# Kernel tuning notes

Measured on AMD Instinct MI355X. Metric: run time of the kernel, lower is better.

## Reference

```python
import jax, jax.numpy as jnp
import numpy as np

B, S, D, H = 4, 2048, 1024, 16
HD = D // H


def setup_inputs() -> dict:
    key = jax.random.key(0)
    ks = jax.random.split(key, 11)
    s = 1.0 / np.sqrt(D)
    return {
        "query": jax.random.normal(ks[0], (B, S, D), jnp.float32),
        "key": jax.random.normal(ks[1], (B, S, D), jnp.float32),
        "value": jax.random.normal(ks[2], (B, S, D), jnp.float32),
        "Wq": jax.random.normal(ks[3], (D, D), jnp.float32) * s,
        "bq": jax.random.normal(ks[4], (D,), jnp.float32) * s,
        "Wk": jax.random.normal(ks[5], (D, D), jnp.float32) * s,
        "bk": jax.random.normal(ks[6], (D,), jnp.float32) * s,
        "Wv": jax.random.normal(ks[7], (D, D), jnp.float32) * s,
        "bv": jax.random.normal(ks[8], (D,), jnp.float32) * s,
        "Wo": jax.random.normal(ks[9], (D, D), jnp.float32) * s,
        "bo": jax.random.normal(ks[10], (D,), jnp.float32) * s,
    }


def reference(query, key, value, Wq, bq, Wk, bk, Wv, bv, Wo, bo):
    b = query.shape[0]
    # projections (torch Linear: x @ W.T + b)
    q = (query @ Wq.T + bq).reshape(b, -1, H, HD).transpose(0, 2, 1, 3)  # [B,H,S,hd]
    k = (key @ Wk.T + bk).reshape(b, -1, H, HD).transpose(0, 2, 1, 3)
    v = (value @ Wv.T + bv).reshape(b, -1, H, HD).transpose(0, 2, 1, 3)
    scores = jnp.einsum('bhqd,bhkd->bhqk', q, k) / jnp.sqrt(jnp.float32(HD))
    attn = jax.nn.softmax(scores, axis=-1)  # dropout = identity (eval)
    out = jnp.einsum('bhqk,bhkd->bhqd', attn, v)
    out = out.transpose(0, 2, 1, 3).reshape(b, -1, D)
    return out @ Wo.T + bo
```

## Files before the change

### kernel.cpp

```cpp
#include <hip/hip_runtime.h>
#include <stdint.h>

typedef __attribute__((ext_vector_type(8))) short  s16x8;
typedef __attribute__((ext_vector_type(4))) float  f32x4;
typedef __attribute__((ext_vector_type(4))) unsigned short u16x4;

__device__ __forceinline__ unsigned short f2bf(float f) {
  union { float f; uint32_t u; } x; x.f = f;
  uint32_t u = x.u;
  return (unsigned short)((u + 0x7fffu + ((u >> 16) & 1u)) >> 16);
}

__device__ __forceinline__ float fexp2(float x) {
  float r; asm("v_exp_f32 %0, %1" : "=v"(r) : "v"(x)); return r;
}
__device__ __forceinline__ uint32_t cvtpk_bf16(float lo, float hi) {
  uint32_t r; asm("v_cvt_pk_bf16_f32 %0, %1, %2" : "=v"(r) : "v"(lo), "v"(hi)); return r;
}

__device__ __forceinline__ void gload_lds16(const void* g, void* l) {
  __builtin_amdgcn_global_load_lds(
      (const __attribute__((address_space(1))) void*)g,
      (__attribute__((address_space(3))) void*)l, 16, 0, 0);
}

struct CvtJobs {
  const float* src[7];
  unsigned short* dst[7];
  int n4[7];
};
__global__ __launch_bounds__(256) void cvt_all(CvtJobs jobs) {
  const int j = blockIdx.y;
  const float* __restrict__ src = jobs.src[j];
  unsigned short* __restrict__ dst = jobs.dst[j];
  const int n4 = jobs.n4[j];
  const int stride = gridDim.x * blockDim.x;
  for (int i = blockIdx.x * blockDim.x + threadIdx.x; i < n4; i += stride) {
    f32x4 v = *(const f32x4*)(src + (size_t)i * 4);
    u16x4 o = { f2bf(v[0]), f2bf(v[1]), f2bf(v[2]), f2bf(v[3]) };
    *(u16x4*)(dst + (size_t)i * 4) = o;
  }
}

struct GemmJob {
  const unsigned short* A;
  const unsigned short* Bmat;
  const float* bias;
  unsigned short* C;
  int M, N, Nb;
  int bias_row;
  float scale;
};

__device__ __forceinline__ void gemm_core(const unsigned short* __restrict__ A,
                                          const unsigned short* __restrict__ Bw,
                                          int m0, int n0, int K,
                                          unsigned short* Al, unsigned short* Bl,
                                          f32x4 (&acc)[4][4]) {
  const int tid = threadIdx.x;
  const int l = tid & 63, w = tid >> 6;
  const int lr = l & 15, lc = l >> 4;
  const int wr = w >> 1, wc = w & 1;
  const int srow = l >> 2, skc = (l & 3) * 8;
  for (int kt = 0; kt < K; kt += 32) {
#pragma unroll
    for (int p = 0; p < 2; ++p) {
      int c = w + 4 * p;
      int row = c * 16 + srow;
      gload_lds16(A + (size_t)(m0 + row) * K + kt + skc, &Al[c * 512 + l * 8]);
      gload_lds16(Bw + (size_t)(n0 + row) * K + kt + skc, &Bl[c * 512 + l * 8]);
    }
    __syncthreads();
    s16x8 af[4], bfr[4];
#pragma unroll
    for (int i = 0; i < 4; ++i)
      af[i] = *(const s16x8*)&Al[(wr * 64 + i * 16 + lr) * 32 + lc * 8];
#pragma unroll
    for (int j = 0; j < 4; ++j)
      bfr[j] = *(const s16x8*)&Bl[(wc * 64 + j * 16 + lr) * 32 + lc * 8];
#pragma unroll
    for (int i = 0; i < 4; ++i)
#pragma unroll
      for (int j = 0; j < 4; ++j)
        acc[i][j] = __builtin_amdgcn_mfma_f32_16x16x32_bf16(af[i], bfr[j], acc[i][j], 0, 0, 0);
    __syncthreads();
  }
}

__global__ __launch_bounds__(256) void gemm_qkv(GemmJob j0, GemmJob j1, GemmJob j2) {
  __shared__ __align__(16) unsigned short Al[4096];
  __shared__ __align__(16) unsigned short Bl[4096];
  const GemmJob jb = (blockIdx.y == 0) ? j0 : (blockIdx.y == 1) ? j1 : j2;
  const int flat = blockIdx.x;
  const int m0 = (flat / jb.Nb) * 128, n0 = (flat % jb.Nb) * 128;
  f32x4 acc[4][4];
#pragma unroll
  for (int i = 0; i < 4; ++i)
#pragma unroll
    for (int j = 0; j < 4; ++j) acc[i][j] = (f32x4){0.f, 0.f, 0.f, 0.f};
  gemm_core(jb.A, jb.Bmat, m0, n0, 1024, Al, Bl, acc);
  const int tid = threadIdx.x;
  const int l = tid & 63, w = tid >> 6;
  const int lr = l & 15, lc = l >> 4;
  const int wr = w >> 1, wc = w & 1;
#pragma unroll
  for (int i = 0; i < 4; ++i) {
    const int row0 = m0 + wr * 64 + i * 16 + lc * 4;
    f32x4 brow;
    if (jb.bias_row) brow = *(const f32x4*)&jb.bias[row0];
#pragma unroll
    for (int j = 0; j < 4; ++j) {
      const int col = n0 + wc * 64 + j * 16 + lr;
      float bcol = jb.bias_row ? 0.f : jb.bias[col];
#pragma unroll
      for (int r = 0; r < 4; ++r) {
        float v = (acc[i][j][r] + (jb.bias_row ? brow[r] : bcol)) * jb.scale;
        jb.C[(size_t)(row0 + r) * jb.N + col] = f2bf(v);
      }
    }
  }
}

__global__ __launch_bounds__(256) void gemm_out(const unsigned short* __restrict__ A,
                                                const unsigned short* __restrict__ Bw,
                                                const float* __restrict__ bias,
                                                float* __restrict__ Cout,
                                                int M, int N, int K) {
  __shared__ __align__(16) unsigned short Al[4096];
  __shared__ __align__(16) unsigned short Bl[4096];
  const int m0 = blockIdx.x * 128, n0 = blockIdx.y * 128;
  f32x4 acc[4][4];
#pragma unroll
  for (int i = 0; i < 4; ++i)
#pragma unroll
    for (int j = 0; j < 4; ++j) acc[i][j] = (f32x4){0.f, 0.f, 0.f, 0.f};
  gemm_core(A, Bw, m0, n0, K, Al, Bl, acc);
  const int tid = threadIdx.x;
  const int l = tid & 63, w = tid >> 6;
  const int lr = l & 15, lc = l >> 4;
  const int wr = w >> 1, wc = w & 1;
#pragma unroll
  for (int i = 0; i < 4; ++i) {
    const int row0 = m0 + wr * 64 + i * 16 + lc * 4;
#pragma unroll
    for (int j = 0; j < 4; ++j) {
      const int col = n0 + wc * 64 + j * 16 + lr;
      float bcol = bias[col];
#pragma unroll
      for (int r = 0; r < 4; ++r)
        Cout[(size_t)(row0 + r) * N + col] = acc[i][j][r] + bcol;
    }
  }
}

__global__ __launch_bounds__(512) void attn_fwd(const unsigned short* __restrict__ qb,
                                                const unsigned short* __restrict__ kb,
                                                const unsigned short* __restrict__ vtb,
                                                unsigned short* __restrict__ ob) {
  __shared__ __align__(16) unsigned short L[3 * 8192];
  const int tid = threadIdx.x;
  const int l = tid & 63, w = tid >> 6;
  const int lr = l & 15, lc = l >> 4;
  const int i0 = blockIdx.x;
  const int wid = (i0 & 7) * 128 + (i0 >> 3);
  const int qx = wid & 15;
  const int h = (wid >> 4) & 15;
  const int b = wid >> 8;
  const int q0 = qx * 128;
  const size_t qkbase = ((size_t)b * 2048) * 1024 + (size_t)h * 64;
  const size_t vtbase = (size_t)(h * 64) * 8192 + (size_t)b * 2048;

  s16x8 aq0, aq1;
  {
    const unsigned short* qp = qb + qkbase + (size_t)(q0 + w * 16 + lr) * 1024 + lc * 8;
    aq0 = *(const s16x8*)qp;
    aq1 = *(const s16x8*)(qp + 32);
  }

  float lsum = 0.f;
  f32x4 oacc[4];
#pragma unroll
  for (int nd = 0; nd < 4; ++nd) oacc[nd] = (f32x4){0.f, 0.f, 0.f, 0.f};

  const int role = w >> 2, wk = w & 3;
  const int rl = l >> 3;
  const int cs = (l & 7) ^ rl;
  const int rA = wk * 16 + rl, rB = rA + 8;
#define RHO(rr) (8 * (((rr) >> 2) & 3) + 4 * (((rr) >> 4) & 1) + ((rr) & 3) + 32 * ((rr) >> 5))
  const unsigned short* sA;
  const unsigned short* sB;
  size_t tstep;
  if (role == 0) {
    sA = kb + qkbase + (size_t)RHO(rA) * 1024 + cs * 8;
    sB = kb + qkbase + (size_t)RHO(rB) * 1024 + cs * 8;
    tstep = (size_t)64 * 1024;
  } else {
    sA = vtb + vtbase + (size_t)rA * 8192 + cs * 8;
    sB = vtb + vtbase + (size_t)rB * 8192 + cs * 8;
    tstep = 64;
  }
#undef RHO
  char* dstL = (char*)L + role * 8192 + wk * 2048 + l * 16;

#define STAGE(BUF, T) {                                              \
    gload_lds16(sA + (size_t)(T) * tstep, dstL + (BUF) * 16384);     \
    gload_lds16(sB + (size_t)(T) * tstep, dstL + (BUF) * 16384 + 1024); }

  int off0[4];
#pragma unroll
  for (int ni = 0; ni < 4; ++ni)
    off0[ni] = (ni * 16 + lr) * 128 + ((lc ^ (lr & 7)) * 16);

  STAGE(0, 0);
  STAGE(1, 1);

  int cur = 0;
  for (int t = 0; t < 32; ++t) {
    if (t < 31) asm volatile("s_waitcnt vmcnt(2)" ::: "memory");
    else        asm volatile("s_waitcnt vmcnt(0)" ::: "memory");
    __builtin_amdgcn_s_barrier();
    if (t < 30) {
      int nb = cur + 2; if (nb >= 3) nb -= 3;
      STAGE(nb, t + 2);
    }
    const char* Lb = (const char*)L + cur * 16384;

    f32x4 sf[4];
    __builtin_amdgcn_s_setprio(1);
#pragma unroll
    for (int ni = 0; ni < 4; ++ni) {
      s16x8 k0 = *(const s16x8*)(Lb + off0[ni]);
      s16x8 k1 = *(const s16x8*)(Lb + (off0[ni] ^ 64));
      f32x4 z = (f32x4){0.f, 0.f, 0.f, 0.f};
      z = __builtin_amdgcn_mfma_f32_16x16x32_bf16(k0, aq0, z, 0, 0, 0);
      z = __builtin_amdgcn_mfma_f32_16x16x32_bf16(k1, aq1, z, 0, 0, 0);
      sf[ni] = z;
    }
    __builtin_amdgcn_s_setprio(0);

    union { uint32_t u[4]; s16x8 v; } pa0u, pa1u;
#pragma unroll
    for (int ni = 0; ni < 4; ++ni) {
      float p0 = fexp2(sf[ni][0]);
      float p1 = fexp2(sf[ni][1]);
      float p2 = fexp2(sf[ni][2]);
      float p3 = fexp2(sf[ni][3]);
      lsum += (p0 + p1) + (p2 + p3);
      uint32_t w0 = cvtpk_bf16(p0, p1);
      uint32_t w1 = cvtpk_bf16(p2, p3);
      if (ni < 2) { pa0u.u[ni * 2] = w0; pa0u.u[ni * 2 + 1] = w1; }
      else        { pa1u.u[(ni - 2) * 2] = w0; pa1u.u[(ni - 2) * 2 + 1] = w1; }
    }

    __builtin_amdgcn_s_setprio(1);
#pragma unroll
    for (int nd = 0; nd < 4; ++nd) {
      s16x8 v0 = *(const s16x8*)(Lb + 8192 + off0[nd]);
      s16x8 v1 = *(const s16x8*)(Lb + 8192 + (off0[nd] ^ 64));
      oacc[nd] = __builtin_amdgcn_mfma_f32_16x16x32_bf16(pa0u.v, v0, oacc[nd], 0, 0, 0);
      oacc[nd] = __builtin_amdgcn_mfma_f32_16x16x32_bf16(pa1u.v, v1, oacc[nd], 0, 0, 0);
    }
    __builtin_amdgcn_s_setprio(0);

    ++cur; if (cur == 3) cur = 0;
  }

  lsum += __shfl_xor(lsum, 16, 64);
  lsum += __shfl_xor(lsum, 32, 64);
  float linv[4];
#pragma unroll
  for (int r = 0; r < 4; ++r) linv[r] = 1.f / __shfl(lsum, lc * 4 + r, 64);
#pragma unroll
  for (int nd = 0; nd < 4; ++nd)
#pragma unroll
    for (int r = 0; r < 4; ++r) {
      int qrow = q0 + w * 16 + lc * 4 + r;
      ob[qkbase + (size_t)qrow * 1024 + nd * 16 + lr] = f2bf(oacc[nd][r] * linv[r]);
    }
#undef STAGE
}

extern "C" void kernel_launch(void* const* d_in, const int* in_sizes, int n_in,
                              void* d_out, int out_size, void* d_ws, size_t ws_size,
                              hipStream_t stream) {
  const float* query = (const float*)d_in[0];
  const float* key_  = (const float*)d_in[1];
  const float* value = (const float*)d_in[2];
  const float* Wq = (const float*)d_in[3];
  const float* bq = (const float*)d_in[4];
  const float* Wk = (const float*)d_in[5];
  const float* bk = (const float*)d_in[6];
  const float* Wv = (const float*)d_in[7];
  const float* bv = (const float*)d_in[8];
  const float* Wo = (const float*)d_in[9];
  const float* bo = (const float*)d_in[10];

  const int MS = 4 * 2048;
  const int D = 1024;
  const size_t NX = (size_t)MS * D;
  const size_t NW = (size_t)D * D;

  const size_t need = (6 * NX + 4 * NW) * 2;
  if (ws_size < need) return;

  unsigned short* ws  = (unsigned short*)d_ws;
  unsigned short* xq  = ws;
  unsigned short* xk  = xq + NX;
  unsigned short* xv  = xk + NX;
  unsigned short* qb_ = xv + NX;
  unsigned short* kb_ = qb_ + NX;
  unsigned short* vtb = kb_ + NX;
  unsigned short* wqb = vtb + NX;
  unsigned short* wkb = wqb + NW;
  unsigned short* wvb = wkb + NW;
  unsigned short* wob = wvb + NW;
  unsigned short* attn = xq;

  CvtJobs cj;
  cj.src[0] = query; cj.dst[0] = xq;  cj.n4[0] = (int)(NX / 4);
  cj.src[1] = key_;  cj.dst[1] = xk;  cj.n4[1] = (int)(NX / 4);
  cj.src[2] = value; cj.dst[2] = xv;  cj.n4[2] = (int)(NX / 4);
  cj.src[3] = Wq;    cj.dst[3] = wqb; cj.n4[3] = (int)(NW / 4);
  cj.src[4] = Wk;    cj.dst[4] = wkb; cj.n4[4] = (int)(NW / 4);
  cj.src[5] = Wv;    cj.dst[5] = wvb; cj.n4[5] = (int)(NW / 4);
  cj.src[6] = Wo;    cj.dst[6] = wob; cj.n4[6] = (int)(NW / 4);
  cvt_all<<<dim3(1024, 7), 256, 0, stream>>>(cj);

  const float qscale = 0.18033688f;
  GemmJob jq = { xq,  wqb, bq, qb_, MS, D,  D / 128,  0, qscale };
  GemmJob jk = { xk,  wkb, bk, kb_, MS, D,  D / 128,  0, 1.f };
  GemmJob jv = { wvb, xv,  bv, vtb, D,  MS, MS / 128, 1, 1.f };
  gemm_qkv<<<dim3(512, 3), 256, 0, stream>>>(jq, jk, jv);

  attn_fwd<<<dim3(1024), 512, 0, stream>>>(qb_, kb_, vtb, attn);

  gemm_out<<<dim3(MS / 128, D / 128), 256, 0, stream>>>(attn, wob, bo, (float*)d_out, MS, D, D);
}
```

Baseline: 215.4 us.

## Pipeline GEMMs with triple-buffered LDS, 8 waves, swizzle and XCD-aware block remap

Replaces the single-buffered, double-barrier GEMM core with a three-stage LDS ring in which global-to-LDS loads for tile t+2 are issued while tile t is computed, using vmcnt waits and one barrier per step. Blocks now have 512 threads (8 waves, each computing a 32x64 sub-tile), the LDS rows are XOR-swizzled to avoid bank conflicts, MFMA sections run at raised priority, and block indices are remapped across the 8 XCDs for cache locality. The intent is to hide memory latency and reduce barrier stalls in the QKV and output projections. In exchange, LDS use rises to 48KB per block and per-wave arithmetic intensity drops.

Measured after the change: 205.4 us. -4.7%, faster.

```diff
diff --git a/kernel.cpp b/kernel.cpp
--- a/kernel.cpp
+++ b/kernel.cpp
@@ -52,96 +52,121 @@
   float scale;
 };
 
-__device__ __forceinline__ void gemm_core(const unsigned short* __restrict__ A,
-                                          const unsigned short* __restrict__ Bw,
-                                          int m0, int n0, int K,
-                                          unsigned short* Al, unsigned short* Bl,
-                                          f32x4 (&acc)[4][4]) {
+__device__ __forceinline__ void gemm_core8(const unsigned short* __restrict__ A,
+                                           const unsigned short* __restrict__ Bw,
+                                           int m0, int n0, int K, char* L,
+                                           f32x4 (&acc)[2][4]) {
+  const int tid = threadIdx.x;
+  const int l = tid & 63;
+  const int lr = l & 15, lc = l >> 4;
+  const int w = tid >> 6;
+  const int wr = w >> 1, wc = w & 1;
+
+  const int srow = tid >> 2;
+  const int sc = (tid & 3) ^ ((srow >> 1) & 3);
+  const unsigned short* sA = A + (size_t)(m0 + srow) * K + sc * 8;
+  const unsigned short* sB = Bw + (size_t)(n0 + srow) * K + sc * 8;
+  char* dA = L + (size_t)tid * 16;
+  char* dB = L + 8192 + (size_t)tid * 16;
+
+#define GSTAGE(BUF, KS) { gload_lds16(sA + (KS), dA + (BUF) * 16384); \
+                          gload_lds16(sB + (KS), dB + (BUF) * 16384); }
+
+  const int s16 = (lc ^ ((lr >> 1) & 3)) * 16;
+  int offA[2], offB[4];
+#pragma unroll
+  for (int i = 0; i < 2; ++i) offA[i] = (wr * 32 + i * 16 + lr) * 64 + s16;
+#pragma unroll
+  for (int j = 0; j < 4; ++j) offB[j] = 8192 + (wc * 64 + j * 16 + lr) * 64 + s16;
+
+  const int nk = K >> 5;
+  GSTAGE(0, 0);
+  GSTAGE(1, 32);
+  int cur = 0;
+  for (int t = 0; t < nk; ++t) {
+    if (t < nk - 1) asm volatile("s_waitcnt vmcnt(2)" ::: "memory");
+    else            asm volatile("s_waitcnt vmcnt(0)" ::: "memory");
+    __builtin_amdgcn_s_barrier();
+    if (t < nk - 2) {
+      int nb = cur + 2; if (nb >= 3) nb -= 3;
+      GSTAGE(nb, (t + 2) * 32);
+    }
+    const char* Lb = L + cur * 16384;
+    s16x8 af[2], bfr[4];
+#pragma unroll
+    for (int i = 0; i < 2; ++i) af[i] = *(const s16x8*)(Lb + offA[i]);
+#pragma unroll
+    for (int j = 0; j < 4; ++j) bfr[j] = *(const s16x8*)(Lb + offB[j]);
+    __builtin_amdgcn_s_setprio(1);
+#pragma unroll
+    for (int i = 0; i < 2; ++i)
+#pragma unroll
+      for (int j = 0; j < 4; ++j)
+        acc[i][j] = __builtin_amdgcn_mfma_f32_16x16x32_bf16(af[i], bfr[j], acc[i][j], 0, 0, 0);
+    __builtin_amdgcn_s_setprio(0);
+    ++cur; if (cur == 3) cur = 0;
+  }
+#undef GSTAGE
+}
+
+__global__ __launch_bounds__(512) void gemm_qkv(GemmJob j0, GemmJob j1, GemmJob j2) {
+  __shared__ __align__(16) char L[49152];
+  const int f = blockIdx.x;
+  const int wid = (f & 7) * 192 + (f >> 3);
+  const int job = wid >> 9;
+  const int i = wid & 511;
+  const GemmJob jb = (job == 0) ? j0 : (job == 1) ? j1 : j2;
+  const int m0 = (i / jb.Nb) * 128, n0 = (i % jb.Nb) * 128;
+  f32x4 acc[2][4];
+#pragma unroll
+  for (int i2 = 0; i2 < 2; ++i2)
+#pragma unroll
+    for (int j2 = 0; j2 < 4; ++j2) acc[i2][j2] = (f32x4){0.f, 0.f, 0.f, 0.f};
+  gemm_core8(jb.A, jb.Bmat, m0, n0, 1024, L, acc);
   const int tid = threadIdx.x;
   const int l = tid & 63, w = tid >> 6;
   const int lr = l & 15, lc = l >> 4;
   const int wr = w >> 1, wc = w & 1;
-  const int srow = l >> 2, skc = (l & 3) * 8;
-  for (int kt = 0; kt < K; kt += 32) {
-#pragma unroll
-    for (int p = 0; p < 2; ++p) {
-      int c = w + 4 * p;
-      int row = c * 16 + srow;
-      gload_lds16(A + (size_t)(m0 + row) * K + kt + skc, &Al[c * 512 + l * 8]);
-      gload_lds16(Bw + (size_t)(n0 + row) * K + kt + skc, &Bl[c * 512 + l * 8]);
-    }
-    __syncthreads();
-    s16x8 af[4], bfr[4];
-#pragma unroll
-    for (int i = 0; i < 4; ++i)
-      af[i] = *(const s16x8*)&Al[(wr * 64 + i * 16 + lr) * 32 + lc * 8];
-#pragma unroll
-    for (int j = 0; j < 4; ++j)
-      bfr[j] = *(const s16x8*)&Bl[(wc * 64 + j * 16 + lr) * 32 + lc * 8];
-#pragma unroll
-    for (int i = 0; i < 4; ++i)
-#pragma unroll
-      for (int j = 0; j < 4; ++j)
-        acc[i][j] = __builtin_amdgcn_mfma_f32_16x16x32_bf16(af[i], bfr[j], acc[i][j], 0, 0, 0);
-    __syncthreads();
-  }
-}
-
-__global__ __launch_bounds__(256) void gemm_qkv(GemmJob j0, GemmJob j1, GemmJob j2) {
-  __shared__ __align__(16) unsigned short Al[4096];
-  __shared__ __align__(16) unsigned short Bl[4096];
-  const GemmJob jb = (blockIdx.y == 0) ? j0 : (blockIdx.y == 1) ? j1 : j2;
-  const int flat = blockIdx.x;
-  const int m0 = (flat / jb.Nb) * 128, n0 = (flat % jb.Nb) * 128;
-  f32x4 acc[4][4];
-#pragma unroll
-  for (int i = 0; i < 4; ++i)
+#pragma unroll
+  for (int i2 = 0; i2 < 2; ++i2) {
+    const int row0 = m0 + wr * 32 + i2 * 16 + lc * 4;
+    f32x4 brow;
+    if (jb.bias_row) brow = *(const f32x4*)&jb.bias[row0];
+#pragma unroll
+    for (int j2 = 0; j2 < 4; ++j2) {
+      const int col = n0 + wc * 64 + j2 * 16 + lr;
+      float bcol = jb.bias_row ? 0.f : jb.bias[col];
+#pragma unroll
+      for (int r = 0; r < 4; ++r) {
+        float v = (acc[i2][j2][r] + (jb.bias_row ? brow[r] : bcol)) * jb.scale;
+        jb.C[(size_t)(row0 + r) * jb.N + col] = f2bf(v);
+      }
+    }
+  }
+}
+
+__global__ __launch_bounds__(512) void gemm_out(const unsigned short* __restrict__ A,
+                                                const unsigned short* __restrict__ Bw,
+                                                const float* __restrict__ bias,
+                                                float* __restrict__ Cout,
+                                                int M, int N, int K) {
+  __shared__ __align__(16) char L[49152];
+  const int f = blockIdx.x;
+  const int wid = (f & 7) * 64 + (f >> 3);
+  const int m0 = (wid >> 3) * 128, n0 = (wid & 7) * 128;
+  f32x4 acc[2][4];
+#pragma unroll
+  for (int i = 0; i < 2; ++i)
 #pragma unroll
     for (int j = 0; j < 4; ++j) acc[i][j] = (f32x4){0.f, 0.f, 0.f, 0.f};
-  gemm_core(jb.A, jb.Bmat, m0, n0, 1024, Al, Bl, acc);
+  gemm_core8(A, Bw, m0, n0, K, L, acc);
   const int tid = threadIdx.x;
   const int l = tid & 63, w = tid >> 6;
   const int lr = l & 15, lc = l >> 4;
   const int wr = w >> 1, wc = w & 1;
 #pragma unroll
-  for (int i = 0; i < 4; ++i) {
-    const int row0 = m0 + wr * 64 + i * 16 + lc * 4;
-    f32x4 brow;
-    if (jb.bias_row) brow = *(const f32x4*)&jb.bias[row0];
-#pragma unroll
-    for (int j = 0; j < 4; ++j) {
-      const int col = n0 + wc * 64 + j * 16 + lr;
-      float bcol = jb.bias_row ? 0.f : jb.bias[col];
-#pragma unroll
-      for (int r = 0; r < 4; ++r) {
-        float v = (acc[i][j][r] + (jb.bias_row ? brow[r] : bcol)) * jb.scale;
-        jb.C[(size_t)(row0 + r) * jb.N + col] = f2bf(v);
-      }
-    }
-  }
-}
-
-__global__ __launch_bounds__(256) void gemm_out(const unsigned short* __restrict__ A,
-                                                const unsigned short* __restrict__ Bw,
-                                                const float* __restrict__ bias,
-                                                float* __restrict__ Cout,
-                                                int M, int N, int K) {
-  __shared__ __align__(16) unsigned short Al[4096];
-  __shared__ __align__(16) unsigned short Bl[4096];
-  const int m0 = blockIdx.x * 128, n0 = blockIdx.y * 128;
-  f32x4 acc[4][4];
-#pragma unroll
-  for (int i = 0; i < 4; ++i)
-#pragma unroll
-    for (int j = 0; j < 4; ++j) acc[i][j] = (f32x4){0.f, 0.f, 0.f, 0.f};
-  gemm_core(A, Bw, m0, n0, K, Al, Bl, acc);
-  const int tid = threadIdx.x;
-  const int l = tid & 63, w = tid >> 6;
-  const int lr = l & 15, lc = l >> 4;
-  const int wr = w >> 1, wc = w & 1;
-#pragma unroll
-  for (int i = 0; i < 4; ++i) {
-    const int row0 = m0 + wr * 64 + i * 16 + lc * 4;
+  for (int i = 0; i < 2; ++i) {
+    const int row0 = m0 + wr * 32 + i * 16 + lc * 4;
 #pragma unroll
     for (int j = 0; j < 4; ++j) {
       const int col = n0 + wc * 64 + j * 16 + lr;
@@ -330,9 +355,9 @@
   GemmJob jq = { xq,  wqb, bq, qb_, MS, D,  D / 128,  0, qscale };
   GemmJob jk = { xk,  wkb, bk, kb_, MS, D,  D / 128,  0, 1.f };
   GemmJob jv = { wvb, xv,  bv, vtb, D,  MS, MS / 128, 1, 1.f };
-  gemm_qkv<<<dim3(512, 3), 256, 0, stream>>>(jq, jk, jv);
+  gemm_qkv<<<dim3(1536), 512, 0, stream>>>(jq, jk, jv);
 
   attn_fwd<<<dim3(1024), 512, 0, stream>>>(qb_, kb_, vtb, attn);
 
-  gemm_out<<<dim3(MS / 128, D / 128), 256, 0, stream>>>(attn, wob, bo, (float*)d_out, MS, D, D);
-}
+  gemm_out<<<dim3(512), 512, 0, stream>>>(attn, wob, bo, (float*)d_out, MS, D, D);
+}
```
